# Performance work log

Hardware: AMD Instinct MI355X
Metric: run time of the kernel (lower is better)

The kernel has to match this reference:

```python
import jax, jax.numpy as jnp
import numpy as np

N_NODES = 50000
N_EDGES = 800000
D = 128
K_HOPS = 2  # ConvLayer k=2 -> k+1=3 accumulated terms


def conv_layer(feat, src, dst, W, b):
    # DGL-style symmetric-norm GCN hop accumulation (method='sum', relu)
    n = feat.shape[0]
    ones = jnp.ones(src.shape[0], dtype=feat.dtype)
    deg = jax.ops.segment_sum(ones, src, num_segments=n)  # out-degrees
    norm = jnp.clip(deg, 1.0, None) ** -0.5  # [N]
    norm = norm[:, None]
    rst = feat @ W + b
    for _ in range(K_HOPS):
        feat = feat * norm
        # update_all(copy_u, sum): gather src features, scatter-sum to dst
        feat = jax.ops.segment_sum(feat[src], dst, num_segments=n)
        feat = feat * norm
        rst = rst + feat @ W + b  # original code reuses weights[0] each hop
    return jax.nn.relu(rst)


def setup_inputs() -> dict:
    key = jax.random.key(0)
    ks = jax.random.split(key, 6)
    xavier = (6.0 / (D + D)) ** 0.5
    feat = jax.random.normal(ks[0], (N_NODES, D), dtype=jnp.float32)
    src = jax.random.randint(ks[1], (N_EDGES,), 0, N_NODES, dtype=jnp.int32)
    dst = jax.random.randint(ks[2], (N_EDGES,), 0, N_NODES, dtype=jnp.int32)
    W1 = jax.random.uniform(ks[3], (D, D), jnp.float32, -xavier, xavier)
    W2 = jax.random.uniform(ks[4], (D, D), jnp.float32, -xavier, xavier)
    b1 = jnp.zeros((D,), jnp.float32)
    b2 = jnp.zeros((D,), jnp.float32)
    return {"feat": feat, "W1": W1, "b1": b1, "W2": W2, "b2": b2,
            "src": src, "dst": dst}


def reference(feat, W1, b1, W2, b2, src, dst):
    # GraphEmbbeding: stacked ConvLayers (num_layers=2)
    h = conv_layer(feat, src, dst, W1, b1)
    h = conv_layer(h, src, dst, W2, b2)
    return h
```

## Files before the change

kernel.cpp:

```cpp
#include <hip/hip_runtime.h>

#define N_NODES 50000
#define N_EDGES 800000
#define D 128
#define NSB ((N_NODES + 255) / 256)
#define NCH 64
#define EPC (N_EDGES / NCH)
#define NR 8
#define RNG (N_NODES / NR)

typedef unsigned short ushort_t;
typedef unsigned int uint_t;
typedef short s16x8 __attribute__((ext_vector_type(8)));
typedef float f32x4 __attribute__((ext_vector_type(4)));

__device__ __forceinline__ float bf2f(ushort_t u) {
    uint_t x = ((uint_t)u) << 16;
    return __builtin_bit_cast(float, x);
}
__device__ __forceinline__ ushort_t f2bf(float f) {
    uint_t u = __builtin_bit_cast(uint_t, f);
    uint_t r = (u + 0x7FFFu + ((u >> 16) & 1u)) >> 16;
    return (ushort_t)r;
}

__global__ __launch_bounds__(256) void kb_hist(const int* __restrict__ src,
        const int* __restrict__ dst, uint_t* __restrict__ hist) {
    __shared__ uint_t h[RNG];
    int chunk = blockIdx.x, range = blockIdx.y;
    int base = range * RNG;
    int t = threadIdx.x;
    for (int i = t; i < RNG; i += 256) h[i] = 0;
    __syncthreads();
    int e0 = chunk * EPC;
    for (int e = e0 + t; e < e0 + EPC; e += 256) {
        unsigned su = (unsigned)(src[e] - base);
        unsigned du = (unsigned)(dst[e] - base);
        if (su < RNG) atomicAdd(&h[su], 1u << 16);
        if (du < RNG) atomicAdd(&h[du], 1u);
    }
    __syncthreads();
    uint_t* oh = hist + (size_t)chunk * N_NODES + base;
    for (int i = t; i < RNG; i += 256) oh[i] = h[i];
}

__global__ void kb_reduce(uint_t* __restrict__ hist, int* __restrict__ indeg,
                          float* __restrict__ norm, float* __restrict__ rnorm) {
    int n = blockIdx.x * 256 + threadIdx.x;
    if (n >= N_NODES) return;
    int run = 0, od = 0;
#pragma unroll
    for (int c = 0; c < NCH; ++c) {
        size_t idx = (size_t)c * N_NODES + n;
        uint_t v = hist[idx];
        hist[idx] = (uint_t)run;
        run += (int)(v & 0xFFFFu);
        od  += (int)(v >> 16);
    }
    indeg[n] = run;
    float dg = fmaxf((float)od, 1.0f);
    norm[n]  = 1.0f / sqrtf(dg);
    rnorm[n] = sqrtf(dg);
}

__global__ void k_scanA(const int* __restrict__ indeg, int* __restrict__ off,
                        int* __restrict__ bsum) {
    __shared__ int sh[256];
    int t = threadIdx.x;
    int i = blockIdx.x * 256 + t;
    int v = (i < N_NODES) ? indeg[i] : 0;
    sh[t] = v;
    __syncthreads();
    for (int d = 1; d < 256; d <<= 1) {
        int x = sh[t];
        int y = (t >= d) ? sh[t - d] : 0;
        __syncthreads();
        sh[t] = x + y;
        __syncthreads();
    }
    if (i < N_NODES) off[i] = sh[t] - v;
    if (t == 255) bsum[blockIdx.x] = sh[255];
}

__global__ void k_scanB(const int* __restrict__ bsum, int* __restrict__ bbase,
                        int* __restrict__ off) {
    __shared__ int sh[256];
    int t = threadIdx.x;
    int v = (t < NSB) ? bsum[t] : 0;
    sh[t] = v;
    __syncthreads();
    for (int d = 1; d < 256; d <<= 1) {
        int x = sh[t];
        int y = (t >= d) ? sh[t - d] : 0;
        __syncthreads();
        sh[t] = x + y;
        __syncthreads();
    }
    if (t < NSB) bbase[t] = sh[t] - v;
    if (t == 255) off[N_NODES] = sh[255];
}

__global__ void k_scanC(int* __restrict__ off, const int* __restrict__ bbase) {
    int i = blockIdx.x * 256 + threadIdx.x;
    if (i < N_NODES) off[i] += bbase[blockIdx.x];
}

__global__ __launch_bounds__(256) void kb_scatter(const int* __restrict__ src,
        const int* __restrict__ dst, const int* __restrict__ off,
        const uint_t* __restrict__ hist, int* __restrict__ csrc) {
    __shared__ int slot[RNG];
    int chunk = blockIdx.x, range = blockIdx.y;
    int base = range * RNG;
    int t = threadIdx.x;
    const uint_t* hb = hist + (size_t)chunk * N_NODES + base;
    for (int i = t; i < RNG; i += 256) slot[i] = off[base + i] + (int)hb[i];
    __syncthreads();
    int e0 = chunk * EPC;
    for (int e = e0 + t; e < e0 + EPC; e += 256) {
        unsigned du = (unsigned)(dst[e] - base);
        if (du < RNG) {
            int p = atomicAdd(&slot[du], 1);
            csrc[p] = src[e];
        }
    }
}

__global__ void k_prepw(const float* __restrict__ W, ushort_t* __restrict__ Wt) {
    int i = blockIdx.x * 256 + threadIdx.x;
    if (i < D * D) {
        int col = i >> 7, k = i & 127;
        Wt[i] = f2bf(W[(size_t)k * D + col]);
    }
}

__global__ void k_init(const float* __restrict__ X, const float* __restrict__ norm,
                       ushort_t* __restrict__ A) {
    int i = blockIdx.x * blockDim.x + threadIdx.x;
    const int total = N_NODES * (D / 4);
    if (i < total) {
        int row = i >> 5;
        float4 v = ((const float4*)X)[i];
        float nm = norm[row];
        ushort4 a = {f2bf(v.x * nm), f2bf(v.y * nm), f2bf(v.z * nm), f2bf(v.w * nm)};
        ((ushort4*)A)[i] = a;
    }
}

__global__ __launch_bounds__(256) void k_prop(const ushort_t* __restrict__ Ain,
                       const int* __restrict__ off, const int* __restrict__ csrc,
                       const float* __restrict__ norm,
                       ushort_t* __restrict__ Aout, int mode) {
    int w = blockIdx.x * 16 + (threadIdx.x >> 4);
    if (w >= N_NODES) return;
    int li = threadIdx.x & 15;
    int s0 = off[w], s1 = off[w + 1];
    float a0=0.f,a1=0.f,a2=0.f,a3=0.f,a4=0.f,a5=0.f,a6=0.f,a7=0.f;
    const s16x8* A8 = (const s16x8*)Ain;
    for (int j = s0; j < s1; j += 8) {
#pragma unroll
        for (int k = 0; k < 8; ++k) {
            int jj = j + k;
            int jc = jj < s1 ? jj : s1 - 1;
            int s = csrc[jc];
            s16x8 v = A8[(size_t)s * 16 + li];
            if (jj < s1) {
                a0 += bf2f((ushort_t)v[0]); a1 += bf2f((ushort_t)v[1]);
                a2 += bf2f((ushort_t)v[2]); a3 += bf2f((ushort_t)v[3]);
                a4 += bf2f((ushort_t)v[4]); a5 += bf2f((ushort_t)v[5]);
                a6 += bf2f((ushort_t)v[6]); a7 += bf2f((ushort_t)v[7]);
            }
        }
    }
    float nm = norm[w];
    float f = mode ? nm : nm * nm;
    s16x8 o;
    o[0] = (short)f2bf(a0 * f); o[1] = (short)f2bf(a1 * f);
    o[2] = (short)f2bf(a2 * f); o[3] = (short)f2bf(a3 * f);
    o[4] = (short)f2bf(a4 * f); o[5] = (short)f2bf(a5 * f);
    o[6] = (short)f2bf(a6 * f); o[7] = (short)f2bf(a7 * f);
    ((s16x8*)Aout)[(size_t)w * 16 + li] = o;
}

__global__ __launch_bounds__(256) void k_gemm_relu(const float* __restrict__ X0,
        const ushort_t* __restrict__ A1, const ushort_t* __restrict__ X2,
        const float* __restrict__ rnorm,
        const ushort_t* __restrict__ Wt, const float* __restrict__ bias,
        float* __restrict__ out, ushort_t* __restrict__ Anext,
        const float* __restrict__ norm, float bscale) {
    __shared__ ushort_t Xs[64 * D];
    __shared__ ushort_t Ws[D * D];
    int t = threadIdx.x;
    int row0 = blockIdx.x * 64;
    const s16x8* Wg = (const s16x8*)Wt;
    s16x8* Ws8 = (s16x8*)Ws;
    for (int i = t; i < D * 16; i += 256) {
        int col = i >> 4, c = i & 15;
        Ws8[(col << 4) | (c ^ (col & 7))] = Wg[i];
    }
    s16x8* Xs8 = (s16x8*)Xs;
    for (int i = t; i < 64 * 16; i += 256) {
        int r = i >> 4, c = i & 15;
        int gr = row0 + r;
        s16x8 ov;
        if (gr < N_NODES) {
            size_t b4 = (size_t)gr * 32 + c * 2;
            float4  x0a = ((const float4*)X0)[b4], x0b = ((const float4*)X0)[b4 + 1];
            ushort4 p0 = ((const ushort4*)A1)[b4], p1 = ((const ushort4*)A1)[b4 + 1];
            ushort4 q0 = ((const ushort4*)X2)[b4], q1 = ((const ushort4*)X2)[b4 + 1];
            float rn = rnorm[gr];
            ov[0] = (short)f2bf(x0a.x + bf2f(p0.x) * rn + bf2f(q0.x));
            ov[1] = (short)f2bf(x0a.y + bf2f(p0.y) * rn + bf2f(q0.y));
            ov[2] = (short)f2bf(x0a.z + bf2f(p0.z) * rn + bf2f(q0.z));
            ov[3] = (short)f2bf(x0a.w + bf2f(p0.w) * rn + bf2f(q0.w));
            ov[4] = (short)f2bf(x0b.x + bf2f(p1.x) * rn + bf2f(q1.x));
            ov[5] = (short)f2bf(x0b.y + bf2f(p1.y) * rn + bf2f(q1.y));
            ov[6] = (short)f2bf(x0b.z + bf2f(p1.z) * rn + bf2f(q1.z));
            ov[7] = (short)f2bf(x0b.w + bf2f(p1.w) * rn + bf2f(q1.w));
        } else {
            ov = (s16x8)0;
        }
        Xs8[(r << 4) | (c ^ (r & 7))] = ov;
    }
    __syncthreads();
    int wid = t >> 6, l = t & 63;
    int lrow = l & 15, lk = l >> 4;
    f32x4 acc[8];
#pragma unroll
    for (int nt = 0; nt < 8; ++nt) acc[nt] = (f32x4){0.f, 0.f, 0.f, 0.f};
    const s16x8* Xr = (const s16x8*)Xs;
    const s16x8* Wr = (const s16x8*)Ws;
#pragma unroll
    for (int ks = 0; ks < 4; ++ks) {
        int kc = ks * 4 + lk;
        int ar = wid * 16 + lrow;
        s16x8 a = Xr[(ar << 4) | (kc ^ (ar & 7))];
#pragma unroll
        for (int nt = 0; nt < 8; ++nt) {
            int bc = nt * 16 + lrow;
            s16x8 b = Wr[(bc << 4) | (kc ^ (bc & 7))];
            acc[nt] = __builtin_amdgcn_mfma_f32_16x16x32_bf16(a, b, acc[nt], 0, 0, 0);
        }
    }
    int rbase = row0 + wid * 16 + lk * 4;
#pragma unroll
    for (int nt = 0; nt < 8; ++nt) {
        int C = nt * 16 + lrow;
        float bv = bias[C] * bscale;
#pragma unroll
        for (int r = 0; r < 4; ++r) {
            int R = rbase + r;
            if (R < N_NODES) {
                float o = fmaxf(acc[nt][r] + bv, 0.f);
                out[(size_t)R * D + C] = o;
                if (Anext) Anext[(size_t)R * D + C] = f2bf(o * norm[R]);
            }
        }
    }
}

extern "C" void kernel_launch(void* const* d_in, const int* in_sizes, int n_in,
                              void* d_out, int out_size, void* d_ws, size_t ws_size,
                              hipStream_t stream) {
    const float* feat = (const float*)d_in[0];
    const float* W1   = (const float*)d_in[1];
    const float* b1   = (const float*)d_in[2];
    const float* W2   = (const float*)d_in[3];
    const float* b2   = (const float*)d_in[4];
    const int*   src  = (const int*)d_in[5];
    const int*   dst  = (const int*)d_in[6];
    float* out = (float*)d_out;

    char* ws = (char*)d_ws;
    size_t o = 0;
    auto alloc = [&](size_t bytes) {
        void* p = ws + o;
        o += (bytes + 1023) & ~(size_t)1023;
        return p;
    };
    uint_t*   hist  = (uint_t*)alloc((size_t)NCH * N_NODES * 4);
    int*      indeg = (int*)alloc(N_NODES * 4);
    float*    norm  = (float*)alloc(N_NODES * 4);
    float*    rnorm = (float*)alloc(N_NODES * 4);
    int*      off   = (int*)alloc((N_NODES + 1) * 4);
    int*      bsum  = (int*)alloc(NSB * 4);
    int*      bbase = (int*)alloc(NSB * 4);
    int*      csrc  = (int*)alloc((size_t)N_EDGES * 4);
    ushort_t* bufA  = (ushort_t*)alloc((size_t)N_NODES * D * 2);
    ushort_t* bufB  = (ushort_t*)alloc((size_t)N_NODES * D * 2);
    ushort_t* bufC  = (ushort_t*)alloc((size_t)N_NODES * D * 2);
    ushort_t* Wt1   = (ushort_t*)alloc((size_t)D * D * 2);
    ushort_t* Wt2   = (ushort_t*)alloc((size_t)D * D * 2);
    (void)ws_size; (void)in_sizes; (void)n_in; (void)out_size;

    kb_hist<<<dim3(NCH, NR), 256, 0, stream>>>(src, dst, hist);
    kb_reduce<<<(N_NODES + 255) / 256, 256, 0, stream>>>(hist, indeg, norm, rnorm);
    k_scanA<<<NSB, 256, 0, stream>>>(indeg, off, bsum);
    k_scanB<<<1, 256, 0, stream>>>(bsum, bbase, off);
    k_scanC<<<NSB, 256, 0, stream>>>(off, bbase);
    kb_scatter<<<dim3(NCH, NR), 256, 0, stream>>>(src, dst, off, hist, csrc);
    k_prepw<<<(D * D + 255) / 256, 256, 0, stream>>>(W1, Wt1);
    k_prepw<<<(D * D + 255) / 256, 256, 0, stream>>>(W2, Wt2);

    const int init_blocks = (N_NODES * 32 + 255) / 256;
    const int prop_blocks = (N_NODES + 15) / 16;
    const int gemm_blocks = (N_NODES + 63) / 64;

    k_init<<<init_blocks, 256, 0, stream>>>(feat, norm, bufA);
    k_prop<<<prop_blocks, 256, 0, stream>>>(bufA, off, csrc, norm, bufB, 0);
    k_prop<<<prop_blocks, 256, 0, stream>>>(bufB, off, csrc, norm, bufC, 1);
    k_gemm_relu<<<gemm_blocks, 256, 0, stream>>>(feat, bufB, bufC, rnorm, Wt1, b1,
                                                 out, bufA, norm, 3.0f);

    k_prop<<<prop_blocks, 256, 0, stream>>>(bufA, off, csrc, norm, bufB, 0);
    k_prop<<<prop_blocks, 256, 0, stream>>>(bufB, off, csrc, norm, bufC, 1);
    k_gemm_relu<<<gemm_blocks, 256, 0, stream>>>(out, bufB, bufC, rnorm, Wt2, b2,
                                                 out, nullptr, norm, 3.0f);
}
```

Before: 280.5 us.

## Batch gather loads in prop, store layer-1 output as bf16, double histogram chunks

The propagation kernel now loads 16 neighbor indices and then 16 feature rows before accumulating, so more gathers are in flight, and it handles the tail with masked FMAs. Its launch bounds now request two blocks per multiprocessor. The first GEMM writes its intermediate output as bf16 into a new buffer instead of fp32 into the output array, which halves that write and the later read. The histogram chunk count is doubled with a partially unrolled reduction. The cost is higher register pressure in prop, and the intermediate layer is stored at reduced precision.

```diff
diff --git a/kernel.cpp b/kernel.cpp
--- a/kernel.cpp
+++ b/kernel.cpp
@@ -4,7 +4,7 @@
 #define N_EDGES 800000
 #define D 128
 #define NSB ((N_NODES + 255) / 256)
-#define NCH 64
+#define NCH 128
 #define EPC (N_EDGES / NCH)
 #define NR 8
 #define RNG (N_NODES / NR)
@@ -49,7 +49,7 @@
     int n = blockIdx.x * 256 + threadIdx.x;
     if (n >= N_NODES) return;
     int run = 0, od = 0;
-#pragma unroll
+#pragma unroll 8
     for (int c = 0; c < NCH; ++c) {
         size_t idx = (size_t)c * N_NODES + n;
         uint_t v = hist[idx];
@@ -146,7 +146,7 @@
     }
 }
 
-__global__ __launch_bounds__(256) void k_prop(const ushort_t* __restrict__ Ain,
+__global__ __launch_bounds__(256, 2) void k_prop(const ushort_t* __restrict__ Ain,
                        const int* __restrict__ off, const int* __restrict__ csrc,
                        const float* __restrict__ norm,
                        ushort_t* __restrict__ Aout, int mode) {
@@ -156,18 +156,45 @@
     int s0 = off[w], s1 = off[w + 1];
     float a0=0.f,a1=0.f,a2=0.f,a3=0.f,a4=0.f,a5=0.f,a6=0.f,a7=0.f;
     const s16x8* A8 = (const s16x8*)Ain;
-    for (int j = s0; j < s1; j += 8) {
-#pragma unroll
-        for (int k = 0; k < 8; ++k) {
-            int jj = j + k;
-            int jc = jj < s1 ? jj : s1 - 1;
-            int s = csrc[jc];
-            s16x8 v = A8[(size_t)s * 16 + li];
-            if (jj < s1) {
-                a0 += bf2f((ushort_t)v[0]); a1 += bf2f((ushort_t)v[1]);
-                a2 += bf2f((ushort_t)v[2]); a3 += bf2f((ushort_t)v[3]);
-                a4 += bf2f((ushort_t)v[4]); a5 += bf2f((ushort_t)v[5]);
-                a6 += bf2f((ushort_t)v[6]); a7 += bf2f((ushort_t)v[7]);
+    int j = s0;
+    for (; j + 16 <= s1; j += 16) {
+        int idx[16];
+#pragma unroll
+        for (int k = 0; k < 16; ++k) idx[k] = csrc[j + k];
+        s16x8 v[16];
+#pragma unroll
+        for (int k = 0; k < 16; ++k) v[k] = A8[(size_t)idx[k] * 16 + li];
+#pragma unroll
+        for (int k = 0; k < 16; ++k) {
+            a0 += bf2f((ushort_t)v[k][0]); a1 += bf2f((ushort_t)v[k][1]);
+            a2 += bf2f((ushort_t)v[k][2]); a3 += bf2f((ushort_t)v[k][3]);
+            a4 += bf2f((ushort_t)v[k][4]); a5 += bf2f((ushort_t)v[k][5]);
+            a6 += bf2f((ushort_t)v[k][6]); a7 += bf2f((ushort_t)v[k][7]);
+        }
+    }
+    if (j < s1) {
+        int e1 = s1 - 1;
+        for (; j < s1; j += 8) {
+            int idx[8]; float wk[8];
+#pragma unroll
+            for (int k = 0; k < 8; ++k) {
+                int jj = j + k;
+                idx[k] = csrc[jj < s1 ? jj : e1];
+                wk[k] = (jj < s1) ? 1.f : 0.f;
+            }
+            s16x8 v[8];
+#pragma unroll
+            for (int k = 0; k < 8; ++k) v[k] = A8[(size_t)idx[k] * 16 + li];
+#pragma unroll
+            for (int k = 0; k < 8; ++k) {
+                a0 = fmaf(wk[k], bf2f((ushort_t)v[k][0]), a0);
+                a1 = fmaf(wk[k], bf2f((ushort_t)v[k][1]), a1);
+                a2 = fmaf(wk[k], bf2f((ushort_t)v[k][2]), a2);
+                a3 = fmaf(wk[k], bf2f((ushort_t)v[k][3]), a3);
+                a4 = fmaf(wk[k], bf2f((ushort_t)v[k][4]), a4);
+                a5 = fmaf(wk[k], bf2f((ushort_t)v[k][5]), a5);
+                a6 = fmaf(wk[k], bf2f((ushort_t)v[k][6]), a6);
+                a7 = fmaf(wk[k], bf2f((ushort_t)v[k][7]), a7);
             }
         }
     }
@@ -181,11 +208,13 @@
     ((s16x8*)Aout)[(size_t)w * 16 + li] = o;
 }
 
-__global__ __launch_bounds__(256) void k_gemm_relu(const float* __restrict__ X0,
+__global__ __launch_bounds__(256) void k_gemm_relu(const float* __restrict__ X0f,
+        const ushort_t* __restrict__ X0h,
         const ushort_t* __restrict__ A1, const ushort_t* __restrict__ X2,
         const float* __restrict__ rnorm,
         const ushort_t* __restrict__ Wt, const float* __restrict__ bias,
-        float* __restrict__ out, ushort_t* __restrict__ Anext,
+        float* __restrict__ outf, ushort_t* __restrict__ Hbf,
+        ushort_t* __restrict__ Anext,
         const float* __restrict__ norm, float bscale) {
     __shared__ ushort_t Xs[64 * D];
     __shared__ ushort_t Ws[D * D];
@@ -204,18 +233,27 @@
         s16x8 ov;
         if (gr < N_NODES) {
             size_t b4 = (size_t)gr * 32 + c * 2;
-            float4  x0a = ((const float4*)X0)[b4], x0b = ((const float4*)X0)[b4 + 1];
+            float x[8];
+            if (X0f) {
+                float4 x0a = ((const float4*)X0f)[b4], x0b = ((const float4*)X0f)[b4 + 1];
+                x[0]=x0a.x; x[1]=x0a.y; x[2]=x0a.z; x[3]=x0a.w;
+                x[4]=x0b.x; x[5]=x0b.y; x[6]=x0b.z; x[7]=x0b.w;
+            } else {
+                ushort4 h0 = ((const ushort4*)X0h)[b4], h1 = ((const ushort4*)X0h)[b4 + 1];
+                x[0]=bf2f(h0.x); x[1]=bf2f(h0.y); x[2]=bf2f(h0.z); x[3]=bf2f(h0.w);
+                x[4]=bf2f(h1.x); x[5]=bf2f(h1.y); x[6]=bf2f(h1.z); x[7]=bf2f(h1.w);
+            }
             ushort4 p0 = ((const ushort4*)A1)[b4], p1 = ((const ushort4*)A1)[b4 + 1];
             ushort4 q0 = ((const ushort4*)X2)[b4], q1 = ((const ushort4*)X2)[b4 + 1];
             float rn = rnorm[gr];
-            ov[0] = (short)f2bf(x0a.x + bf2f(p0.x) * rn + bf2f(q0.x));
-            ov[1] = (short)f2bf(x0a.y + bf2f(p0.y) * rn + bf2f(q0.y));
-            ov[2] = (short)f2bf(x0a.z + bf2f(p0.z) * rn + bf2f(q0.z));
-            ov[3] = (short)f2bf(x0a.w + bf2f(p0.w) * rn + bf2f(q0.w));
-            ov[4] = (short)f2bf(x0b.x + bf2f(p1.x) * rn + bf2f(q1.x));
-            ov[5] = (short)f2bf(x0b.y + bf2f(p1.y) * rn + bf2f(q1.y));
-            ov[6] = (short)f2bf(x0b.z + bf2f(p1.z) * rn + bf2f(q1.z));
-            ov[7] = (short)f2bf(x0b.w + bf2f(p1.w) * rn + bf2f(q1.w));
+            ov[0] = (short)f2bf(x[0] + bf2f(p0.x) * rn + bf2f(q0.x));
+            ov[1] = (short)f2bf(x[1] + bf2f(p0.y) * rn + bf2f(q0.y));
+            ov[2] = (short)f2bf(x[2] + bf2f(p0.z) * rn + bf2f(q0.z));
+            ov[3] = (short)f2bf(x[3] + bf2f(p0.w) * rn + bf2f(q0.w));
+            ov[4] = (short)f2bf(x[4] + bf2f(p1.x) * rn + bf2f(q1.x));
+            ov[5] = (short)f2bf(x[5] + bf2f(p1.y) * rn + bf2f(q1.y));
+            ov[6] = (short)f2bf(x[6] + bf2f(p1.z) * rn + bf2f(q1.z));
+            ov[7] = (short)f2bf(x[7] + bf2f(p1.w) * rn + bf2f(q1.w));
         } else {
             ov = (s16x8)0;
         }
@@ -251,8 +289,10 @@
             int R = rbase + r;
             if (R < N_NODES) {
                 float o = fmaxf(acc[nt][r] + bv, 0.f);
-                out[(size_t)R * D + C] = o;
-                if (Anext) Anext[(size_t)R * D + C] = f2bf(o * norm[R]);
+                size_t oi = (size_t)R * D + C;
+                if (outf) outf[oi] = o;
+                if (Hbf) Hbf[oi] = f2bf(o);
+                if (Anext) Anext[oi] = f2bf(o * norm[R]);
             }
         }
     }
@@ -288,6 +328,7 @@
     ushort_t* bufA  = (ushort_t*)alloc((size_t)N_NODES * D * 2);
     ushort_t* bufB  = (ushort_t*)alloc((size_t)N_NODES * D * 2);
     ushort_t* bufC  = (ushort_t*)alloc((size_t)N_NODES * D * 2);
+    ushort_t* bufD  = (ushort_t*)alloc((size_t)N_NODES * D * 2);
     ushort_t* Wt1   = (ushort_t*)alloc((size_t)D * D * 2);
     ushort_t* Wt2   = (ushort_t*)alloc((size_t)D * D * 2);
     (void)ws_size; (void)in_sizes; (void)n_in; (void)out_size;
@@ -308,11 +349,11 @@
     k_init<<<init_blocks, 256, 0, stream>>>(feat, norm, bufA);
     k_prop<<<prop_blocks, 256, 0, stream>>>(bufA, off, csrc, norm, bufB, 0);
     k_prop<<<prop_blocks, 256, 0, stream>>>(bufB, off, csrc, norm, bufC, 1);
-    k_gemm_relu<<<gemm_blocks, 256, 0, stream>>>(feat, bufB, bufC, rnorm, Wt1, b1,
-                                                 out, bufA, norm, 3.0f);
+    k_gemm_relu<<<gemm_blocks, 256, 0, stream>>>(feat, nullptr, bufB, bufC, rnorm,
+                                                 Wt1, b1, nullptr, bufD, bufA, norm, 3.0f);
 
     k_prop<<<prop_blocks, 256, 0, stream>>>(bufA, off, csrc, norm, bufB, 0);
     k_prop<<<prop_blocks, 256, 0, stream>>>(bufB, off, csrc, norm, bufC, 1);
-    k_gemm_relu<<<gemm_blocks, 256, 0, stream>>>(out, bufB, bufC, rnorm, Wt2, b2,
-                                                 out, nullptr, norm, 3.0f);
-}
+    k_gemm_relu<<<gemm_blocks, 256, 0, stream>>>(nullptr, bufD, bufB, bufC, rnorm,
+                                                 Wt2, b2, out, nullptr, nullptr, norm, 3.0f);
+}
```

After: 227.3 us. 1.23x faster.
